# Optimization experiments

Hardware: AMD Instinct MI355X
Metric: run time of the kernel (lower is better)

Reference implementation:

```python
import jax, jax.numpy as jnp
import numpy as np

N_NODES = 50000
N_EDGES = 500000
N_GRAPH = 128
F_IN = 16
LATENT = 128
STEPS = 3
MLP_LAYERS = 2
OUT_G = 10
LN_EPS = 1e-6


def setup_inputs() -> dict:
    key = jax.random.key(0)
    ks = jax.random.split(key, 8)
    x = jax.random.normal(ks[0], (N_NODES, F_IN), jnp.float32)
    senders = jax.random.randint(ks[1], (N_EDGES,), 0, N_NODES)
    receivers = jax.random.randint(ks[2], (N_EDGES,), 0, N_NODES)
    graph_ids = jnp.sort(jax.random.randint(ks[3], (N_NODES,), 0, N_GRAPH))
    W_embed = jax.random.normal(ks[4], (F_IN, LATENT), jnp.float32) / np.sqrt(F_IN)
    b_embed = jnp.zeros((LATENT,), jnp.float32)
    W_mlp = jax.random.normal(ks[5], (STEPS, MLP_LAYERS, LATENT, LATENT), jnp.float32) / np.sqrt(LATENT)
    b_mlp = jnp.zeros((STEPS, MLP_LAYERS, LATENT), jnp.float32)
    ln_scale = jnp.ones((STEPS, LATENT), jnp.float32)
    ln_bias = jnp.zeros((STEPS, LATENT), jnp.float32)
    W_dec = jax.random.normal(ks[6], (LATENT, OUT_G), jnp.float32) / np.sqrt(LATENT)
    b_dec = jnp.zeros((OUT_G,), jnp.float32)
    return dict(x=x, senders=senders, receivers=receivers, graph_ids=graph_ids,
                W_embed=W_embed, b_embed=b_embed, W_mlp=W_mlp, b_mlp=b_mlp,
                ln_scale=ln_scale, ln_bias=ln_bias, W_dec=W_dec, b_dec=b_dec)


def _layernorm(h, scale, bias):
    mu = jnp.mean(h, axis=-1, keepdims=True)
    var = jnp.mean(jnp.square(h - mu), axis=-1, keepdims=True)
    return (h - mu) * jax.lax.rsqrt(var + LN_EPS) * scale + bias


def reference(x, senders, receivers, graph_ids, W_embed, b_embed,
              W_mlp, b_mlp, ln_scale, ln_bias, W_dec, b_dec):
    N = x.shape[0]
    # node embedder (classical stand-in for quantum node_embedder)
    h = x @ W_embed + b_embed  # [N, latent]

    # add self edges (jraph.GraphConvolution add_self_edges=True)
    self_idx = jnp.arange(N)
    s = jnp.concatenate([senders, self_idx])
    r = jnp.concatenate([receivers, self_idx])
    ones = jnp.ones(s.shape, h.dtype)
    inv_sqrt_deg_s = jax.lax.rsqrt(jnp.maximum(jax.ops.segment_sum(ones, s, N), 1.0))[:, None]
    inv_sqrt_deg_r = jax.lax.rsqrt(jnp.maximum(jax.ops.segment_sum(ones, r, N), 1.0))[:, None]

    for t in range(STEPS):
        # per-node MLP update (Dense + tanh per layer)
        u = h
        for l in range(MLP_LAYERS):
            u = jnp.tanh(u @ W_mlp[t, l] + b_mlp[t, l])
        # symmetric-normalized segment-sum aggregation
        u = u * inv_sqrt_deg_s
        u = jax.ops.segment_sum(u[s], r, N)
        u = u * inv_sqrt_deg_r
        # skip connection + layernorm
        h = u + h
        h = _layernorm(h, ln_scale[t], ln_bias[t])

    # segment-mean pooling over graphs
    counts = jax.ops.segment_sum(jnp.ones((N,), h.dtype), graph_ids, N_GRAPH)
    pooled = jax.ops.segment_sum(h, graph_ids, N_GRAPH) / jnp.maximum(counts, 1.0)[:, None]
    # global decoder
    return pooled @ W_dec + b_dec  # [N_GRAPH, OUT_G]
```

## Files before the change

### kernel.cpp

```cpp
#include <hip/hip_runtime.h>
#include <hip/hip_bf16.h>

#define N_NODES 50000
#define N_EDGES 500000
#define N_GRAPH 128
#define F_IN    16
#define LATENT  128
#define STEPS   3
#define LN_EPS  1e-6f
#define OUT_G   10
#define CAP     48

#define PREP_TOTAL 26428

typedef __attribute__((ext_vector_type(8))) short bf16x8;
typedef __attribute__((ext_vector_type(4))) float f32x4;

__device__ __forceinline__ ushort bf16_rtne(float x) {
    uint u = __float_as_uint(x);
    return (ushort)((u + 0x7FFFu + ((u >> 16) & 1u)) >> 16);
}
__device__ __forceinline__ float bf16_tof(ushort h) {
    return __uint_as_float(((uint)h) << 16);
}
__device__ __forceinline__ float fast_tanh(float x) {
    float t = __expf(x + x);
    return 1.0f - 2.0f * __builtin_amdgcn_rcpf(t + 1.0f);
}
__device__ __forceinline__ void acc4(float4& a, uint2 t, float w) {
    a.x = fmaf(bf16_tof((ushort)(t.x & 0xffffu)), w, a.x);
    a.y = fmaf(bf16_tof((ushort)(t.x >> 16)),     w, a.y);
    a.z = fmaf(bf16_tof((ushort)(t.y & 0xffffu)), w, a.z);
    a.w = fmaf(bf16_tof((ushort)(t.y >> 16)),     w, a.w);
}

__global__ __launch_bounds__(256) void prep_fused(const int* __restrict__ s,
                                                  const int* __restrict__ r,
                                                  int* __restrict__ cnt_r,
                                                  int* __restrict__ cnt_s,
                                                  ushort* __restrict__ bucket,
                                                  const float* __restrict__ x,
                                                  const float* __restrict__ We,
                                                  const float* __restrict__ be,
                                                  ushort* __restrict__ h_hi,
                                                  ushort* __restrict__ h_lo,
                                                  const float* __restrict__ Wm,
                                                  ushort* __restrict__ w_hi,
                                                  ushort* __restrict__ w_lo,
                                                  const int* __restrict__ gids,
                                                  int* __restrict__ gstart,
                                                  float* __restrict__ pooled) {
    const int bid = blockIdx.x;
    const int tid = threadIdx.x;

    if (bid % 27 == 0) {
        int eidx = bid / 27;
        int e0 = (eidx * 256 + tid) * 2;
        if (e0 < N_EDGES) {
            int2 ss = *reinterpret_cast<const int2*>(&s[e0]);
            int2 rr = *reinterpret_cast<const int2*>(&r[e0]);
            int sl0 = atomicAdd(&cnt_r[rr.x], 1);
            int sl1 = atomicAdd(&cnt_r[rr.y], 1);
            if (sl0 < CAP) bucket[rr.x * CAP + sl0] = (ushort)ss.x;
            if (sl1 < CAP) bucket[rr.y * CAP + sl1] = (ushort)ss.y;
            atomicAdd(&cnt_s[ss.x], 1);
            atomicAdd(&cnt_s[ss.y], 1);
        }
        return;
    }
    int nidx = bid - bid / 27 - 1;

    if (nidx < 25000) {
        int idx = nidx * 256 + tid;
        int n = idx >> 7, j = idx & 127;
        float sacc = be[j];
        #pragma unroll
        for (int k = 0; k < F_IN; ++k) sacc = fmaf(x[n * F_IN + k], We[k * LATENT + j], sacc);
        ushort hi = bf16_rtne(sacc);
        h_hi[idx] = hi;
        h_lo[idx] = bf16_rtne(sacc - bf16_tof(hi));
    } else if (nidx < 25384) {
        int idx = (nidx - 25000) * 256 + tid;
        int tl = idx >> 14, rem = idx & 16383, j = rem >> 7, k = rem & 127;
        float w = Wm[(tl << 14) + k * 128 + j];
        ushort hi = bf16_rtne(w);
        w_hi[idx] = hi;
        w_lo[idx] = bf16_rtne(w - bf16_tof(hi));
    } else if (nidx < 25448) {
        pooled[(nidx - 25384) * 256 + tid] = 0.0f;
    } else {
        if (tid <= N_GRAPH) {
            int lo = 0, hi = N_NODES;
            while (lo < hi) { int m = (lo + hi) >> 1; if (gids[m] < tid) lo = m + 1; else hi = m; }
            gstart[tid] = lo;
        }
    }
}

__global__ __launch_bounds__(256) void deg_fin(const int* __restrict__ cnt_s,
                                               const int* __restrict__ cnt_r,
                                               float* __restrict__ inv_s,
                                               float* __restrict__ inv_r, int N) {
    int i = blockIdx.x * 256 + threadIdx.x;
    if (i < N) {
        inv_s[i] = 1.0f / sqrtf((float)(cnt_s[i] + 1));
        inv_r[i] = 1.0f / sqrtf((float)(cnt_r[i] + 1));
    }
}

__global__ __launch_bounds__(256) void mlp_mfma(const ushort* __restrict__ hsp_hi,
                                                const ushort* __restrict__ hsp_lo,
                                                const ushort* __restrict__ wth,
                                                const ushort* __restrict__ wtl,
                                                const float* __restrict__ b0,
                                                const float* __restrict__ b1,
                                                const float* __restrict__ inv_s,
                                                ushort* __restrict__ v16, int N) {
    __shared__ ushort sh_hi[32][136];
    __shared__ ushort sh_lo[32][136];
    const int tid = threadIdx.x;
    const int base = blockIdx.x * 32;

    #pragma unroll
    for (int it = 0; it < 2; ++it) {
        int chunk = it * 256 + tid;
        int row = chunk >> 4, c8 = (chunk & 15) * 8;
        int node = base + row;
        uint4 dh = make_uint4(0, 0, 0, 0), dl = make_uint4(0, 0, 0, 0);
        if (node < N) {
            dh = *reinterpret_cast<const uint4*>(&hsp_hi[node * 128 + c8]);
            dl = *reinterpret_cast<const uint4*>(&hsp_lo[node * 128 + c8]);
        }
        *reinterpret_cast<uint4*>(&sh_hi[row][c8]) = dh;
        *reinterpret_cast<uint4*>(&sh_lo[row][c8]) = dl;
    }
    __syncthreads();

    const int lane = tid & 63;
    const int wv = tid >> 6;
    const int lrow = lane & 15;
    const int lk = (lane >> 4) * 8;
    const int c0 = wv * 32;
    const int crow0 = (lane >> 4) * 4;

    f32x4 acc[2][2];

    {
        float bb0 = b0[c0 + lrow], bb1 = b0[c0 + 16 + lrow];
        #pragma unroll
        for (int rt = 0; rt < 2; ++rt) {
            acc[rt][0] = (f32x4){bb0, bb0, bb0, bb0};
            acc[rt][1] = (f32x4){bb1, bb1, bb1, bb1};
        }
        #pragma unroll
        for (int kt = 0; kt < 4; ++kt) {
            int kk = kt * 32 + lk;
            bf16x8 bh0 = *reinterpret_cast<const bf16x8*>(&wth[(c0 + lrow) * 128 + kk]);
            bf16x8 bl0 = *reinterpret_cast<const bf16x8*>(&wtl[(c0 + lrow) * 128 + kk]);
            bf16x8 bh1 = *reinterpret_cast<const bf16x8*>(&wth[(c0 + 16 + lrow) * 128 + kk]);
            bf16x8 bl1 = *reinterpret_cast<const bf16x8*>(&wtl[(c0 + 16 + lrow) * 128 + kk]);
            #pragma unroll
            for (int rt = 0; rt < 2; ++rt) {
                bf16x8 ah = *reinterpret_cast<const bf16x8*>(&sh_hi[rt * 16 + lrow][kk]);
                bf16x8 al = *reinterpret_cast<const bf16x8*>(&sh_lo[rt * 16 + lrow][kk]);
                acc[rt][0] = __builtin_amdgcn_mfma_f32_16x16x32_bf16(ah, bh0, acc[rt][0], 0, 0, 0);
                acc[rt][0] = __builtin_amdgcn_mfma_f32_16x16x32_bf16(al, bh0, acc[rt][0], 0, 0, 0);
                acc[rt][0] = __builtin_amdgcn_mfma_f32_16x16x32_bf16(ah, bl0, acc[rt][0], 0, 0, 0);
                acc[rt][1] = __builtin_amdgcn_mfma_f32_16x16x32_bf16(ah, bh1, acc[rt][1], 0, 0, 0);
                acc[rt][1] = __builtin_amdgcn_mfma_f32_16x16x32_bf16(al, bh1, acc[rt][1], 0, 0, 0);
                acc[rt][1] = __builtin_amdgcn_mfma_f32_16x16x32_bf16(ah, bl1, acc[rt][1], 0, 0, 0);
            }
        }
    }
    __syncthreads();

    #pragma unroll
    for (int rt = 0; rt < 2; ++rt) {
        #pragma unroll
        for (int ct = 0; ct < 2; ++ct) {
            int col = c0 + ct * 16 + lrow;
            #pragma unroll
            for (int r = 0; r < 4; ++r) {
                float uval = fast_tanh(acc[rt][ct][r]);
                int row = rt * 16 + crow0 + r;
                ushort uh = bf16_rtne(uval);
                ushort ul = bf16_rtne(uval - bf16_tof(uh));
                sh_hi[row][col] = uh;
                sh_lo[row][col] = ul;
            }
        }
    }
    __syncthreads();

    {
        const ushort* w2h = wth + 128 * 128;
        const ushort* w2l = wtl + 128 * 128;
        float bb0 = b1[c0 + lrow], bb1 = b1[c0 + 16 + lrow];
        #pragma unroll
        for (int rt = 0; rt < 2; ++rt) {
            acc[rt][0] = (f32x4){bb0, bb0, bb0, bb0};
            acc[rt][1] = (f32x4){bb1, bb1, bb1, bb1};
        }
        #pragma unroll
        for (int kt = 0; kt < 4; ++kt) {
            int kk = kt * 32 + lk;
            bf16x8 bh0 = *reinterpret_cast<const bf16x8*>(&w2h[(c0 + lrow) * 128 + kk]);
            bf16x8 bl0 = *reinterpret_cast<const bf16x8*>(&w2l[(c0 + lrow) * 128 + kk]);
            bf16x8 bh1 = *reinterpret_cast<const bf16x8*>(&w2h[(c0 + 16 + lrow) * 128 + kk]);
            bf16x8 bl1 = *reinterpret_cast<const bf16x8*>(&w2l[(c0 + 16 + lrow) * 128 + kk]);
            #pragma unroll
            for (int rt = 0; rt < 2; ++rt) {
                bf16x8 ah = *reinterpret_cast<const bf16x8*>(&sh_hi[rt * 16 + lrow][kk]);
                bf16x8 al = *reinterpret_cast<const bf16x8*>(&sh_lo[rt * 16 + lrow][kk]);
                acc[rt][0] = __builtin_amdgcn_mfma_f32_16x16x32_bf16(ah, bh0, acc[rt][0], 0, 0, 0);
                acc[rt][0] = __builtin_amdgcn_mfma_f32_16x16x32_bf16(al, bh0, acc[rt][0], 0, 0, 0);
                acc[rt][0] = __builtin_amdgcn_mfma_f32_16x16x32_bf16(ah, bl0, acc[rt][0], 0, 0, 0);
                acc[rt][1] = __builtin_amdgcn_mfma_f32_16x16x32_bf16(ah, bh1, acc[rt][1], 0, 0, 0);
                acc[rt][1] = __builtin_amdgcn_mfma_f32_16x16x32_bf16(al, bh1, acc[rt][1], 0, 0, 0);
                acc[rt][1] = __builtin_amdgcn_mfma_f32_16x16x32_bf16(ah, bl1, acc[rt][1], 0, 0, 0);
            }
        }
    }

    #pragma unroll
    for (int rt = 0; rt < 2; ++rt) {
        #pragma unroll
        for (int r = 0; r < 4; ++r) {
            int row = rt * 16 + crow0 + r;
            int node = base + row;
            if (node < N) {
                float is = inv_s[node];
                v16[node * 128 + c0 + lrow]      = bf16_rtne(fast_tanh(acc[rt][0][r]) * is);
                v16[node * 128 + c0 + 16 + lrow] = bf16_rtne(fast_tanh(acc[rt][1][r]) * is);
            }
        }
    }
}

__global__ __launch_bounds__(256) void agg_ln_kernel(const ushort* __restrict__ v16,
                                                     const int* __restrict__ cnt_r,
                                                     const ushort* __restrict__ bucket,
                                                     const float* __restrict__ inv_r,
                                                     const float* __restrict__ ln_scale,
                                                     const float* __restrict__ ln_bias,
                                                     ushort* __restrict__ h_hi,
                                                     ushort* __restrict__ h_lo) {
    int lane = threadIdx.x & 63;
    int wave = threadIdx.x >> 6;
    int half = lane >> 5;
    int l32  = lane & 31;
    int hb   = lane & 32;
    int n = blockIdx.x * 8 + wave * 2 + half;
    int c0 = l32 * 4;

    const uint2* vu2 = reinterpret_cast<const uint2*>(v16);

    int deg = cnt_r[n];
    deg = deg < CAP ? deg : CAP;
    int degOther = __shfl_xor(deg, 32);
    int degMin = deg < degOther ? deg : degOther;
    int degMax = deg > degOther ? deg : degOther;

    int my = (l32 < deg) ? (int)bucket[n * CAP + l32] : n;

    float ir = inv_r[n];
    ushort4 hh = *reinterpret_cast<const ushort4*>(&h_hi[n * 128 + c0]);
    ushort4 hl = *reinterpret_cast<const ushort4*>(&h_lo[n * 128 + c0]);
    uint2 selfv = vu2[n * 32 + l32];
    float4 acc = make_float4(0.f, 0.f, 0.f, 0.f);
    acc4(acc, selfv, 1.0f);

    int dm = degMin < 32 ? degMin : 32;
    int dx = degMax < 32 ? degMax : 32;
    int k = 0;
    for (; k + 8 <= dm; k += 8) {
        int src[8]; uint2 t[8];
        #pragma unroll
        for (int j = 0; j < 8; ++j) src[j] = __shfl(my, hb + k + j);
        #pragma unroll
        for (int j = 0; j < 8; ++j) t[j] = vu2[src[j] * 32 + l32];
        #pragma unroll
        for (int j = 0; j < 8; ++j) acc4(acc, t[j], 1.0f);
    }
    for (; k < dx; k += 8) {
        int src[8]; uint2 t[8];
        #pragma unroll
        for (int j = 0; j < 8; ++j) {
            int kj = k + j; kj = kj < 31 ? kj : 31;
            src[j] = __shfl(my, hb + kj);
        }
        #pragma unroll
        for (int j = 0; j < 8; ++j) t[j] = vu2[src[j] * 32 + l32];
        #pragma unroll
        for (int j = 0; j < 8; ++j) acc4(acc, t[j], (k + j < deg) ? 1.0f : 0.0f);
    }
    if (degMax > 32) {
        int my2 = (l32 + 32 < deg) ? (int)bucket[n * CAP + 32 + l32] : n;
        for (int k2 = 32; k2 < degMax; k2 += 8) {
            int src[8]; uint2 t[8];
            #pragma unroll
            for (int j = 0; j < 8; ++j) {
                int kj = k2 + j - 32; kj = kj < 15 ? kj : 15;
                src[j] = __shfl(my2, hb + kj);
            }
            #pragma unroll
            for (int j = 0; j < 8; ++j) t[j] = vu2[src[j] * 32 + l32];
            #pragma unroll
            for (int j = 0; j < 8; ++j) acc4(acc, t[j], (k2 + j < deg) ? 1.0f : 0.0f);
        }
    }

    float4 vv;
    vv.x = fmaf(acc.x, ir, bf16_tof(hh.x) + bf16_tof(hl.x));
    vv.y = fmaf(acc.y, ir, bf16_tof(hh.y) + bf16_tof(hl.y));
    vv.z = fmaf(acc.z, ir, bf16_tof(hh.z) + bf16_tof(hl.z));
    vv.w = fmaf(acc.w, ir, bf16_tof(hh.w) + bf16_tof(hl.w));

    float sred = (vv.x + vv.y) + (vv.z + vv.w);
    #pragma unroll
    for (int off = 16; off; off >>= 1) sred += __shfl_xor(sred, off);
    float mu = sred * (1.0f / 128.0f);
    float dx0 = vv.x - mu, dy0 = vv.y - mu, dz0 = vv.z - mu, dw0 = vv.w - mu;
    float q = (dx0 * dx0 + dy0 * dy0) + (dz0 * dz0 + dw0 * dw0);
    #pragma unroll
    for (int off = 16; off; off >>= 1) q += __shfl_xor(q, off);
    float rs = 1.0f / sqrtf(q * (1.0f / 128.0f) + LN_EPS);

    float4 ls = *reinterpret_cast<const float4*>(&ln_scale[c0]);
    float4 lb = *reinterpret_cast<const float4*>(&ln_bias[c0]);
    float o0 = fmaf(dx0 * rs, ls.x, lb.x);
    float o1 = fmaf(dy0 * rs, ls.y, lb.y);
    float o2 = fmaf(dz0 * rs, ls.z, lb.z);
    float o3 = fmaf(dw0 * rs, ls.w, lb.w);
    ushort h0 = bf16_rtne(o0), h1 = bf16_rtne(o1), h2 = bf16_rtne(o2), h3 = bf16_rtne(o3);
    ushort l0 = bf16_rtne(o0 - bf16_tof(h0)), l1 = bf16_rtne(o1 - bf16_tof(h1));
    ushort l2 = bf16_rtne(o2 - bf16_tof(h2)), l3 = bf16_rtne(o3 - bf16_tof(h3));
    ushort4 oh; oh.x = h0; oh.y = h1; oh.z = h2; oh.w = h3;
    ushort4 ol; ol.x = l0; ol.y = l1; ol.z = l2; ol.w = l3;
    *reinterpret_cast<ushort4*>(&h_hi[n * 128 + c0]) = oh;
    *reinterpret_cast<ushort4*>(&h_lo[n * 128 + c0]) = ol;
}

__global__ __launch_bounds__(128) void pool_partial(const ushort* __restrict__ h_hi,
                                                    const ushort* __restrict__ h_lo,
                                                    const int* __restrict__ gstart,
                                                    float* __restrict__ pooled) {
    int g = blockIdx.x >> 3;
    int sidx = blockIdx.x & 7;
    int start = gstart[g], end = gstart[g + 1];
    int len = end - start;
    int c0 = start + (len * sidx) / 8;
    int c1 = start + (len * (sidx + 1)) / 8;
    if (c1 <= c0) return;
    int j = threadIdx.x;
    float sacc = 0.0f;
    for (int n = c0; n < c1; ++n)
        sacc += bf16_tof(h_hi[n * 128 + j]) + bf16_tof(h_lo[n * 128 + j]);
    atomicAdd(&pooled[g * 128 + j], sacc);
}

__global__ __launch_bounds__(128) void decode_kernel(const float* __restrict__ pooled,
                                                     const int* __restrict__ gstart,
                                                     const float* __restrict__ W_dec,
                                                     const float* __restrict__ b_dec,
                                                     float* __restrict__ out) {
    __shared__ float pl[128];
    int g = blockIdx.x;
    int cnt = gstart[g + 1] - gstart[g];
    float inv = 1.0f / (float)max(cnt, 1);
    pl[threadIdx.x] = pooled[g * 128 + threadIdx.x] * inv;
    __syncthreads();
    if (threadIdx.x < OUT_G) {
        int o = threadIdx.x;
        float sacc = b_dec[o];
        for (int jj = 0; jj < 128; ++jj) sacc = fmaf(pl[jj], W_dec[jj * OUT_G + o], sacc);
        out[g * OUT_G + o] = sacc;
    }
}

extern "C" void kernel_launch(void* const* d_in, const int* in_sizes, int n_in,
                              void* d_out, int out_size, void* d_ws, size_t ws_size,
                              hipStream_t stream) {
    const float* x        = (const float*)d_in[0];
    const int*   senders  = (const int*)d_in[1];
    const int*   receivers= (const int*)d_in[2];
    const int*   gids     = (const int*)d_in[3];
    const float* W_embed  = (const float*)d_in[4];
    const float* b_embed  = (const float*)d_in[5];
    const float* W_mlp    = (const float*)d_in[6];
    const float* b_mlp    = (const float*)d_in[7];
    const float* ln_scale = (const float*)d_in[8];
    const float* ln_bias  = (const float*)d_in[9];
    const float* W_dec    = (const float*)d_in[10];
    const float* b_dec    = (const float*)d_in[11];
    float* out = (float*)d_out;

    const int N = N_NODES;
    char* ws = (char*)d_ws;
    size_t off = 0;
    auto alloc = [&](size_t bytes) { size_t o = off; off = (off + bytes + 255) & ~(size_t)255; return o; };
    ushort* h_hi    = (ushort*)(ws + alloc((size_t)N * 128 * 2));
    ushort* h_lo    = (ushort*)(ws + alloc((size_t)N * 128 * 2));
    ushort* v16     = (ushort*)(ws + alloc((size_t)N * 128 * 2));
    int*   cnts     = (int*)  (ws + alloc((size_t)2 * N * 4));
    int*   cnt_r    = cnts;
    int*   cnt_s    = cnts + N;
    float* inv_s    = (float*)(ws + alloc((size_t)N * 4));
    float* inv_r    = (float*)(ws + alloc((size_t)N * 4));
    ushort* bucket  = (ushort*)(ws + alloc((size_t)N * CAP * 2));
    float* pooled   = (float*)(ws + alloc((size_t)N_GRAPH * 128 * 4));
    int*   gstart   = (int*)  (ws + alloc((size_t)(N_GRAPH + 1) * 4));
    ushort* w_hi    = (ushort*)(ws + alloc((size_t)STEPS * 2 * 128 * 128 * 2));
    ushort* w_lo    = (ushort*)(ws + alloc((size_t)STEPS * 2 * 128 * 128 * 2));

    hipMemsetAsync(cnts, 0, (size_t)2 * N * 4, stream);
    prep_fused<<<PREP_TOTAL, 256, 0, stream>>>(senders, receivers, cnt_r, cnt_s, bucket,
                                               x, W_embed, b_embed, h_hi, h_lo,
                                               W_mlp, w_hi, w_lo, gids, gstart, pooled);
    deg_fin<<<(N + 255) / 256, 256, 0, stream>>>(cnt_s, cnt_r, inv_s, inv_r, N);

    for (int t = 0; t < STEPS; ++t) {
        const ushort* wth = w_hi + (size_t)t * 2 * 128 * 128;
        const ushort* wtl = w_lo + (size_t)t * 2 * 128 * 128;
        const float* bb0 = b_mlp + (size_t)(t * 2 + 0) * 128;
        const float* bb1 = b_mlp + (size_t)(t * 2 + 1) * 128;
        mlp_mfma<<<(N + 31) / 32, 256, 0, stream>>>(h_hi, h_lo, wth, wtl, bb0, bb1, inv_s, v16, N);
        agg_ln_kernel<<<N / 8, 256, 0, stream>>>(v16, cnt_r, bucket, inv_r,
                                                 ln_scale + t * 128, ln_bias + t * 128, h_hi, h_lo);
    }

    pool_partial <<<N_GRAPH * 8, 128, 0, stream>>>(h_hi, h_lo, gstart, pooled);
    decode_kernel<<<N_GRAPH, 128, 0, stream>>>(pooled, gstart, W_dec, b_dec, out);
}
```

Measured before the change: 337.1 us.

## Fuse aggregation+layernorm with next step's MLP and inline degree normalisation

Fuses step t's aggregation and layernorm with step t+1's MLP in one kernel. The normalised h rows go straight into LDS as the MLP input, so h is not re-read from global memory between kernels. v buffers are double-buffered (v_a/v_b) because the fused kernel reads the previous v and writes the new one. The deg_fin kernel and the inv_s/inv_r arrays are removed, with rsqrt of the degree counts computed inline instead. This saves several launches and a global round trip of h, but the fused kernel now pays the gather latency of 32 nodes per block before its MFMA phase, which may hurt occupancy or overlap.

```diff
diff --git a/kernel.cpp b/kernel.cpp
--- a/kernel.cpp
+++ b/kernel.cpp
@@ -12,6 +12,7 @@
 #define CAP     48
 
 #define PREP_TOTAL 26428
+#define MLP_GRID   1563
 
 typedef __attribute__((ext_vector_type(8))) short bf16x8;
 typedef __attribute__((ext_vector_type(4))) float f32x4;
@@ -97,45 +98,121 @@
     }
 }
 
-__global__ __launch_bounds__(256) void deg_fin(const int* __restrict__ cnt_s,
-                                               const int* __restrict__ cnt_r,
-                                               float* __restrict__ inv_s,
-                                               float* __restrict__ inv_r, int N) {
-    int i = blockIdx.x * 256 + threadIdx.x;
-    if (i < N) {
-        inv_s[i] = 1.0f / sqrtf((float)(cnt_s[i] + 1));
-        inv_r[i] = 1.0f / sqrtf((float)(cnt_r[i] + 1));
-    }
-}
-
-__global__ __launch_bounds__(256) void mlp_mfma(const ushort* __restrict__ hsp_hi,
-                                                const ushort* __restrict__ hsp_lo,
-                                                const ushort* __restrict__ wth,
-                                                const ushort* __restrict__ wtl,
-                                                const float* __restrict__ b0,
-                                                const float* __restrict__ b1,
-                                                const float* __restrict__ inv_s,
-                                                ushort* __restrict__ v16, int N) {
-    __shared__ ushort sh_hi[32][136];
-    __shared__ ushort sh_lo[32][136];
-    const int tid = threadIdx.x;
-    const int base = blockIdx.x * 32;
-
-    #pragma unroll
-    for (int it = 0; it < 2; ++it) {
-        int chunk = it * 256 + tid;
-        int row = chunk >> 4, c8 = (chunk & 15) * 8;
-        int node = base + row;
-        uint4 dh = make_uint4(0, 0, 0, 0), dl = make_uint4(0, 0, 0, 0);
-        if (node < N) {
-            dh = *reinterpret_cast<const uint4*>(&hsp_hi[node * 128 + c8]);
-            dl = *reinterpret_cast<const uint4*>(&hsp_lo[node * 128 + c8]);
-        }
-        *reinterpret_cast<uint4*>(&sh_hi[row][c8]) = dh;
-        *reinterpret_cast<uint4*>(&sh_lo[row][c8]) = dl;
-    }
-    __syncthreads();
-
+template<bool TO_LDS>
+__device__ __forceinline__ void agg_pair(const ushort* __restrict__ v_in,
+                                         const int* __restrict__ cnt_r,
+                                         const ushort* __restrict__ bucket,
+                                         const float* __restrict__ ln_scale,
+                                         const float* __restrict__ ln_bias,
+                                         ushort* __restrict__ h_hi,
+                                         ushort* __restrict__ h_lo,
+                                         ushort (*sh_hi)[136], ushort (*sh_lo)[136],
+                                         int n, int row, int l32, int hb) {
+    bool valid = (n < N_NODES);
+    int nc = valid ? n : 0;
+    int c0 = l32 * 4;
+    const uint2* vu2 = reinterpret_cast<const uint2*>(v_in);
+
+    int rawdeg = valid ? cnt_r[nc] : 0;
+    float ir = 1.0f / sqrtf((float)(rawdeg + 1));
+    int deg = rawdeg < CAP ? rawdeg : CAP;
+    int degOther = __shfl_xor(deg, 32);
+    int degMin = deg < degOther ? deg : degOther;
+    int degMax = deg > degOther ? deg : degOther;
+
+    int my = (l32 < deg) ? (int)bucket[nc * CAP + l32] : nc;
+
+    ushort4 hh = *reinterpret_cast<const ushort4*>(&h_hi[nc * 128 + c0]);
+    ushort4 hl = *reinterpret_cast<const ushort4*>(&h_lo[nc * 128 + c0]);
+    uint2 selfv = vu2[nc * 32 + l32];
+    float4 acc = make_float4(0.f, 0.f, 0.f, 0.f);
+    acc4(acc, selfv, 1.0f);
+
+    int dm = degMin < 32 ? degMin : 32;
+    int dxm = degMax < 32 ? degMax : 32;
+    int k = 0;
+    for (; k + 8 <= dm; k += 8) {
+        int src[8]; uint2 t[8];
+        #pragma unroll
+        for (int j = 0; j < 8; ++j) src[j] = __shfl(my, hb + k + j);
+        #pragma unroll
+        for (int j = 0; j < 8; ++j) t[j] = vu2[src[j] * 32 + l32];
+        #pragma unroll
+        for (int j = 0; j < 8; ++j) acc4(acc, t[j], 1.0f);
+    }
+    for (; k < dxm; k += 8) {
+        int src[8]; uint2 t[8];
+        #pragma unroll
+        for (int j = 0; j < 8; ++j) {
+            int kj = k + j; kj = kj < 31 ? kj : 31;
+            src[j] = __shfl(my, hb + kj);
+        }
+        #pragma unroll
+        for (int j = 0; j < 8; ++j) t[j] = vu2[src[j] * 32 + l32];
+        #pragma unroll
+        for (int j = 0; j < 8; ++j) acc4(acc, t[j], (k + j < deg) ? 1.0f : 0.0f);
+    }
+    if (degMax > 32) {
+        int my2 = (l32 + 32 < deg) ? (int)bucket[nc * CAP + 32 + l32] : nc;
+        for (int k2 = 32; k2 < degMax; k2 += 8) {
+            int src[8]; uint2 t[8];
+            #pragma unroll
+            for (int j = 0; j < 8; ++j) {
+                int kj = k2 + j - 32; kj = kj < 15 ? kj : 15;
+                src[j] = __shfl(my2, hb + kj);
+            }
+            #pragma unroll
+            for (int j = 0; j < 8; ++j) t[j] = vu2[src[j] * 32 + l32];
+            #pragma unroll
+            for (int j = 0; j < 8; ++j) acc4(acc, t[j], (k2 + j < deg) ? 1.0f : 0.0f);
+        }
+    }
+
+    float4 vv;
+    vv.x = fmaf(acc.x, ir, bf16_tof(hh.x) + bf16_tof(hl.x));
+    vv.y = fmaf(acc.y, ir, bf16_tof(hh.y) + bf16_tof(hl.y));
+    vv.z = fmaf(acc.z, ir, bf16_tof(hh.z) + bf16_tof(hl.z));
+    vv.w = fmaf(acc.w, ir, bf16_tof(hh.w) + bf16_tof(hl.w));
+
+    float sred = (vv.x + vv.y) + (vv.z + vv.w);
+    #pragma unroll
+    for (int off = 16; off; off >>= 1) sred += __shfl_xor(sred, off);
+    float mu = sred * (1.0f / 128.0f);
+    float dx0 = vv.x - mu, dy0 = vv.y - mu, dz0 = vv.z - mu, dw0 = vv.w - mu;
+    float q = (dx0 * dx0 + dy0 * dy0) + (dz0 * dz0 + dw0 * dw0);
+    #pragma unroll
+    for (int off = 16; off; off >>= 1) q += __shfl_xor(q, off);
+    float rs = 1.0f / sqrtf(q * (1.0f / 128.0f) + LN_EPS);
+
+    float4 ls = *reinterpret_cast<const float4*>(&ln_scale[c0]);
+    float4 lb = *reinterpret_cast<const float4*>(&ln_bias[c0]);
+    float o0 = fmaf(dx0 * rs, ls.x, lb.x);
+    float o1 = fmaf(dy0 * rs, ls.y, lb.y);
+    float o2 = fmaf(dz0 * rs, ls.z, lb.z);
+    float o3 = fmaf(dw0 * rs, ls.w, lb.w);
+    ushort p0 = bf16_rtne(o0), p1 = bf16_rtne(o1), p2 = bf16_rtne(o2), p3 = bf16_rtne(o3);
+    ushort q0 = bf16_rtne(o0 - bf16_tof(p0)), q1 = bf16_rtne(o1 - bf16_tof(p1));
+    ushort q2 = bf16_rtne(o2 - bf16_tof(p2)), q3 = bf16_rtne(o3 - bf16_tof(p3));
+    ushort4 oh; oh.x = p0; oh.y = p1; oh.z = p2; oh.w = p3;
+    ushort4 ol; ol.x = q0; ol.y = q1; ol.z = q2; ol.w = q3;
+    if (valid) {
+        *reinterpret_cast<ushort4*>(&h_hi[n * 128 + c0]) = oh;
+        *reinterpret_cast<ushort4*>(&h_lo[n * 128 + c0]) = ol;
+        if (TO_LDS) {
+            *reinterpret_cast<ushort4*>(&sh_hi[row][c0]) = oh;
+            *reinterpret_cast<ushort4*>(&sh_lo[row][c0]) = ol;
+        }
+    }
+}
+
+__device__ __forceinline__ void mlp_core(ushort (*sh_hi)[136], ushort (*sh_lo)[136],
+                                         const ushort* __restrict__ wth,
+                                         const ushort* __restrict__ wtl,
+                                         const float* __restrict__ b0,
+                                         const float* __restrict__ b1,
+                                         const int* __restrict__ cnt_s,
+                                         ushort* __restrict__ v_out,
+                                         int base, int tid) {
     const int lane = tid & 63;
     const int wv = tid >> 6;
     const int lrow = lane & 15;
@@ -228,117 +305,87 @@
         for (int r = 0; r < 4; ++r) {
             int row = rt * 16 + crow0 + r;
             int node = base + row;
-            if (node < N) {
-                float is = inv_s[node];
-                v16[node * 128 + c0 + lrow]      = bf16_rtne(fast_tanh(acc[rt][0][r]) * is);
-                v16[node * 128 + c0 + 16 + lrow] = bf16_rtne(fast_tanh(acc[rt][1][r]) * is);
+            if (node < N_NODES) {
+                float is = 1.0f / sqrtf((float)(cnt_s[node] + 1));
+                v_out[node * 128 + c0 + lrow]      = bf16_rtne(fast_tanh(acc[rt][0][r]) * is);
+                v_out[node * 128 + c0 + 16 + lrow] = bf16_rtne(fast_tanh(acc[rt][1][r]) * is);
             }
         }
     }
 }
 
-__global__ __launch_bounds__(256) void agg_ln_kernel(const ushort* __restrict__ v16,
+__global__ __launch_bounds__(256) void mlp0_kernel(const ushort* __restrict__ h_hi,
+                                                   const ushort* __restrict__ h_lo,
+                                                   const ushort* __restrict__ wth,
+                                                   const ushort* __restrict__ wtl,
+                                                   const float* __restrict__ b0,
+                                                   const float* __restrict__ b1,
+                                                   const int* __restrict__ cnt_s,
+                                                   ushort* __restrict__ v_out) {
+    __shared__ ushort sh_hi[32][136];
+    __shared__ ushort sh_lo[32][136];
+    const int tid = threadIdx.x;
+    const int base = blockIdx.x * 32;
+    #pragma unroll
+    for (int it = 0; it < 2; ++it) {
+        int chunk = it * 256 + tid;
+        int row = chunk >> 4, c8 = (chunk & 15) * 8;
+        int node = base + row;
+        uint4 dh = make_uint4(0, 0, 0, 0), dl = make_uint4(0, 0, 0, 0);
+        if (node < N_NODES) {
+            dh = *reinterpret_cast<const uint4*>(&h_hi[node * 128 + c8]);
+            dl = *reinterpret_cast<const uint4*>(&h_lo[node * 128 + c8]);
+        }
+        *reinterpret_cast<uint4*>(&sh_hi[row][c8]) = dh;
+        *reinterpret_cast<uint4*>(&sh_lo[row][c8]) = dl;
+    }
+    __syncthreads();
+    mlp_core(sh_hi, sh_lo, wth, wtl, b0, b1, cnt_s, v_out, base, tid);
+}
+
+__global__ __launch_bounds__(256) void fused_agg_mlp(const ushort* __restrict__ v_in,
                                                      const int* __restrict__ cnt_r,
+                                                     const int* __restrict__ cnt_s,
                                                      const ushort* __restrict__ bucket,
-                                                     const float* __restrict__ inv_r,
-                                                     const float* __restrict__ ln_scale,
-                                                     const float* __restrict__ ln_bias,
+                                                     const float* __restrict__ lns,
+                                                     const float* __restrict__ lnb,
+                                                     const ushort* __restrict__ wth,
+                                                     const ushort* __restrict__ wtl,
+                                                     const float* __restrict__ b0,
+                                                     const float* __restrict__ b1,
                                                      ushort* __restrict__ h_hi,
-                                                     ushort* __restrict__ h_lo) {
-    int lane = threadIdx.x & 63;
-    int wave = threadIdx.x >> 6;
-    int half = lane >> 5;
-    int l32  = lane & 31;
-    int hb   = lane & 32;
+                                                     ushort* __restrict__ h_lo,
+                                                     ushort* __restrict__ v_out) {
+    __shared__ ushort sh_hi[32][136];
+    __shared__ ushort sh_lo[32][136];
+    const int tid = threadIdx.x;
+    const int lane = tid & 63, wave = tid >> 6;
+    const int half = lane >> 5, l32 = lane & 31, hb = lane & 32;
+    const int base = blockIdx.x * 32;
+
+    #pragma unroll
+    for (int p = 0; p < 4; ++p) {
+        int row = wave * 8 + p * 2 + half;
+        agg_pair<true>(v_in, cnt_r, bucket, lns, lnb, h_hi, h_lo,
+                       sh_hi, sh_lo, base + row, row, l32, hb);
+    }
+    __syncthreads();
+    mlp_core(sh_hi, sh_lo, wth, wtl, b0, b1, cnt_s, v_out, base, tid);
+}
+
+__global__ __launch_bounds__(256) void agg_final(const ushort* __restrict__ v_in,
+                                                 const int* __restrict__ cnt_r,
+                                                 const ushort* __restrict__ bucket,
+                                                 const float* __restrict__ lns,
+                                                 const float* __restrict__ lnb,
+                                                 ushort* __restrict__ h_hi,
+                                                 ushort* __restrict__ h_lo) {
+    const int tid = threadIdx.x;
+    const int lane = tid & 63, wave = tid >> 6;
+    const int half = lane >> 5, l32 = lane & 31, hb = lane & 32;
     int n = blockIdx.x * 8 + wave * 2 + half;
-    int c0 = l32 * 4;
-
-    const uint2* vu2 = reinterpret_cast<const uint2*>(v16);
-
-    int deg = cnt_r[n];
-    deg = deg < CAP ? deg : CAP;
-    int degOther = __shfl_xor(deg, 32);
-    int degMin = deg < degOther ? deg : degOther;
-    int degMax = deg > degOther ? deg : degOther;
-
-    int my = (l32 < deg) ? (int)bucket[n * CAP + l32] : n;
-
-    float ir = inv_r[n];
-    ushort4 hh = *reinterpret_cast<const ushort4*>(&h_hi[n * 128 + c0]);
-    ushort4 hl = *reinterpret_cast<const ushort4*>(&h_lo[n * 128 + c0]);
-    uint2 selfv = vu2[n * 32 + l32];
-    float4 acc = make_float4(0.f, 0.f, 0.f, 0.f);
-    acc4(acc, selfv, 1.0f);
-
-    int dm = degMin < 32 ? degMin : 32;
-    int dx = degMax < 32 ? degMax : 32;
-    int k = 0;
-    for (; k + 8 <= dm; k += 8) {
-        int src[8]; uint2 t[8];
-        #pragma unroll
-        for (int j = 0; j < 8; ++j) src[j] = __shfl(my, hb + k + j);
-        #pragma unroll
-        for (int j = 0; j < 8; ++j) t[j] = vu2[src[j] * 32 + l32];
-        #pragma unroll
-        for (int j = 0; j < 8; ++j) acc4(acc, t[j], 1.0f);
-    }
-    for (; k < dx; k += 8) {
-        int src[8]; uint2 t[8];
-        #pragma unroll
-        for (int j = 0; j < 8; ++j) {
-            int kj = k + j; kj = kj < 31 ? kj : 31;
-            src[j] = __shfl(my, hb + kj);
-        }
-        #pragma unroll
-        for (int j = 0; j < 8; ++j) t[j] = vu2[src[j] * 32 + l32];
-        #pragma unroll
-        for (int j = 0; j < 8; ++j) acc4(acc, t[j], (k + j < deg) ? 1.0f : 0.0f);
-    }
-    if (degMax > 32) {
-        int my2 = (l32 + 32 < deg) ? (int)bucket[n * CAP + 32 + l32] : n;
-        for (int k2 = 32; k2 < degMax; k2 += 8) {
-            int src[8]; uint2 t[8];
-            #pragma unroll
-            for (int j = 0; j < 8; ++j) {
-                int kj = k2 + j - 32; kj = kj < 15 ? kj : 15;
-                src[j] = __shfl(my2, hb + kj);
-            }
-            #pragma unroll
-            for (int j = 0; j < 8; ++j) t[j] = vu2[src[j] * 32 + l32];
-            #pragma unroll
-            for (int j = 0; j < 8; ++j) acc4(acc, t[j], (k2 + j < deg) ? 1.0f : 0.0f);
-        }
-    }
-
-    float4 vv;
-    vv.x = fmaf(acc.x, ir, bf16_tof(hh.x) + bf16_tof(hl.x));
-    vv.y = fmaf(acc.y, ir, bf16_tof(hh.y) + bf16_tof(hl.y));
-    vv.z = fmaf(acc.z, ir, bf16_tof(hh.z) + bf16_tof(hl.z));
-    vv.w = fmaf(acc.w, ir, bf16_tof(hh.w) + bf16_tof(hl.w));
-
-    float sred = (vv.x + vv.y) + (vv.z + vv.w);
-    #pragma unroll
-    for (int off = 16; off; off >>= 1) sred += __shfl_xor(sred, off);
-    float mu = sred * (1.0f / 128.0f);
-    float dx0 = vv.x - mu, dy0 = vv.y - mu, dz0 = vv.z - mu, dw0 = vv.w - mu;
-    float q = (dx0 * dx0 + dy0 * dy0) + (dz0 * dz0 + dw0 * dw0);
-    #pragma unroll
-    for (int off = 16; off; off >>= 1) q += __shfl_xor(q, off);
-    float rs = 1.0f / sqrtf(q * (1.0f / 128.0f) + LN_EPS);
-
-    float4 ls = *reinterpret_cast<const float4*>(&ln_scale[c0]);
-    float4 lb = *reinterpret_cast<const float4*>(&ln_bias[c0]);
-    float o0 = fmaf(dx0 * rs, ls.x, lb.x);
-    float o1 = fmaf(dy0 * rs, ls.y, lb.y);
-    float o2 = fmaf(dz0 * rs, ls.z, lb.z);
-    float o3 = fmaf(dw0 * rs, ls.w, lb.w);
-    ushort h0 = bf16_rtne(o0), h1 = bf16_rtne(o1), h2 = bf16_rtne(o2), h3 = bf16_rtne(o3);
-    ushort l0 = bf16_rtne(o0 - bf16_tof(h0)), l1 = bf16_rtne(o1 - bf16_tof(h1));
-    ushort l2 = bf16_rtne(o2 - bf16_tof(h2)), l3 = bf16_rtne(o3 - bf16_tof(h3));
-    ushort4 oh; oh.x = h0; oh.y = h1; oh.z = h2; oh.w = h3;
-    ushort4 ol; ol.x = l0; ol.y = l1; ol.z = l2; ol.w = l3;
-    *reinterpret_cast<ushort4*>(&h_hi[n * 128 + c0]) = oh;
-    *reinterpret_cast<ushort4*>(&h_lo[n * 128 + c0]) = ol;
+    agg_pair<false>(v_in, cnt_r, bucket, lns, lnb, h_hi, h_lo,
+                    (ushort(*)[136])nullptr, (ushort(*)[136])nullptr, n, 0, l32, hb);
 }
 
 __global__ __launch_bounds__(128) void pool_partial(const ushort* __restrict__ h_hi,
@@ -401,12 +448,11 @@
     auto alloc = [&](size_t bytes) { size_t o = off; off = (off + bytes + 255) & ~(size_t)255; return o; };
     ushort* h_hi    = (ushort*)(ws + alloc((size_t)N * 128 * 2));
     ushort* h_lo    = (ushort*)(ws + alloc((size_t)N * 128 * 2));
-    ushort* v16     = (ushort*)(ws + alloc((size_t)N * 128 * 2));
+    ushort* v_a     = (ushort*)(ws + alloc((size_t)N * 128 * 2));
+    ushort* v_b     = (ushort*)(ws + alloc((size_t)N * 128 * 2));
     int*   cnts     = (int*)  (ws + alloc((size_t)2 * N * 4));
     int*   cnt_r    = cnts;
     int*   cnt_s    = cnts + N;
-    float* inv_s    = (float*)(ws + alloc((size_t)N * 4));
-    float* inv_r    = (float*)(ws + alloc((size_t)N * 4));
     ushort* bucket  = (ushort*)(ws + alloc((size_t)N * CAP * 2));
     float* pooled   = (float*)(ws + alloc((size_t)N_GRAPH * 128 * 4));
     int*   gstart   = (int*)  (ws + alloc((size_t)(N_GRAPH + 1) * 4));
@@ -417,17 +463,21 @@
     prep_fused<<<PREP_TOTAL, 256, 0, stream>>>(senders, receivers, cnt_r, cnt_s, bucket,
                                                x, W_embed, b_embed, h_hi, h_lo,
                                                W_mlp, w_hi, w_lo, gids, gstart, pooled);
-    deg_fin<<<(N + 255) / 256, 256, 0, stream>>>(cnt_s, cnt_r, inv_s, inv_r, N);
-
-    for (int t = 0; t < STEPS; ++t) {
-        const ushort* wth = w_hi + (size_t)t * 2 * 128 * 128;
-        const ushort* wtl = w_lo + (size_t)t * 2 * 128 * 128;
-        const float* bb0 = b_mlp + (size_t)(t * 2 + 0) * 128;
-        const float* bb1 = b_mlp + (size_t)(t * 2 + 1) * 128;
-        mlp_mfma<<<(N + 31) / 32, 256, 0, stream>>>(h_hi, h_lo, wth, wtl, bb0, bb1, inv_s, v16, N);
-        agg_ln_kernel<<<N / 8, 256, 0, stream>>>(v16, cnt_r, bucket, inv_r,
-                                                 ln_scale + t * 128, ln_bias + t * 128, h_hi, h_lo);
-    }
+
+    mlp0_kernel<<<MLP_GRID, 256, 0, stream>>>(h_hi, h_lo, w_hi, w_lo,
+                                              b_mlp, b_mlp + 128, cnt_s, v_a);
+    fused_agg_mlp<<<MLP_GRID, 256, 0, stream>>>(v_a, cnt_r, cnt_s, bucket,
+                                                ln_scale, ln_bias,
+                                                w_hi + 2 * 16384, w_lo + 2 * 16384,
+                                                b_mlp + 2 * 128, b_mlp + 3 * 128,
+                                                h_hi, h_lo, v_b);
+    fused_agg_mlp<<<MLP_GRID, 256, 0, stream>>>(v_b, cnt_r, cnt_s, bucket,
+                                                ln_scale + 128, ln_bias + 128,
+                                                w_hi + 4 * 16384, w_lo + 4 * 16384,
+                                                b_mlp + 4 * 128, b_mlp + 5 * 128,
+                                                h_hi, h_lo, v_a);
+    agg_final<<<N / 8, 256, 0, stream>>>(v_a, cnt_r, bucket,
+                                         ln_scale + 256, ln_bias + 256, h_hi, h_lo);
 
     pool_partial <<<N_GRAPH * 8, 128, 0, stream>>>(h_hi, h_lo, gstart, pooled);
     decode_kernel<<<N_GRAPH, 128, 0, stream>>>(pooled, gstart, W_dec, b_dec, out);
```

Result: no change. 335.8 us (median of 2 runs) (-0.4%).
